# Optimization experiments

Hardware: AMD Instinct MI355X
Metric: run time of the kernel (lower is better)

## Reference

```python
import jax, jax.numpy as jnp
import numpy as np

B, TK, NK, H, E, V = 128, 400, 50, 256, 256, 50000


def setup_inputs() -> dict:
    key = jax.random.key(0)
    ks = iter(jax.random.split(key, 48))
    def rn(shape, s=1.0):
        return jax.random.normal(next(ks), shape, jnp.float32) * s
    def ru(shape):
        return jax.random.uniform(next(ks), shape, jnp.float32)
    z = lambda shape: jnp.zeros(shape, jnp.float32)
    s = 0.05
    inp = {}
    inp['y_t_1'] = jax.random.randint(next(ks), (B,), 0, V)
    inp['h_prev'] = rn((B, H))
    inp['c_prev'] = rn((B, H))
    inp['encoder_outputs'] = rn((B, TK, H))
    inp['encoder_outputs_node'] = rn((B, NK, H))
    inp['enc_padding_mask'] = jnp.ones((B, TK), jnp.float32)
    inp['enc_padding_mask_node'] = jnp.ones((B, NK), jnp.float32)
    inp['c_t_d'] = rn((B, H))
    inp['c_t_g'] = rn((B, H))
    inp['c_t_g2'] = rn((B, H))
    inp['coverage'] = z((B, TK))
    inp['flow'] = ru((B, NK))
    inp['node_to_token'] = ru((B, NK, TK))
    inp['graph'] = ru((B, NK, NK))
    inp['voc_d'] = jax.random.randint(next(ks), (B, TK), 0, V)
    inp['step'] = 0
    # learned parameters
    inp['emb_table'] = rn((V, E), s)
    inp['Wx'] = rn((4 * H, E), s); inp['bx'] = z((E,))
    inp['Wi'] = rn((E, 4 * H), s); inp['Wh'] = rn((H, 4 * H), s)
    inp['bi'] = z((4 * H,)); inp['bh'] = z((4 * H,))
    inp['Whd'] = rn((H, H), s); inp['Wsd'] = rn((2 * H, H), s)
    inp['wcd'] = rn((H,), s); inp['vd'] = rn((H,), s); inp['bd'] = z((H,))
    inp['Wn'] = rn((H, H), s); inp['Wsf'] = rn((2 * H, H), s)
    inp['vf'] = rn((H,), s); inp['bf'] = z((H,))
    inp['Wpg'] = rn((5 * H + E, 1), s); inp['bpg'] = z((1,))
    inp['W1'] = rn((4 * H, H), s); inp['b1'] = z((H,))
    inp['W2'] = rn((H, V), s); inp['b2'] = z((V,))
    return inp


def _forward(y_t_1, h_prev, c_prev, enc, enc_n, mask_t, mask_n, c_t_d, c_t_g, c_t_g2,
             coverage, flow, n2t, graph, voc_d, emb_table, Wx, bx, Wi, Wh, bi, bh,
             Whd, Wsd, wcd, vd, bd, Wn, Wsf, vf, bf, Wpg, bpg, W1, b1, W2, b2):
    sig, tanh = jax.nn.sigmoid, jnp.tanh
    y_emb = emb_table[y_t_1]                                   # [B,E]
    x = jnp.concatenate([c_t_d, c_t_g, c_t_g2, y_emb], 1) @ Wx + bx
    # single-step LSTM (torch gate order i,f,g,o)
    gates = x @ Wi + h_prev @ Wh + bi + bh
    gi, gf, gg, go = jnp.split(gates, 4, axis=1)
    c_new = sig(gf) * c_prev + sig(gi) * tanh(gg)
    h_new = sig(go) * tanh(c_new)
    s_hat = jnp.concatenate([h_new, c_new], 1)                 # [B,2H]
    # doc attention with coverage (Bahdanau)
    e = tanh(enc @ Whd + (s_hat @ Wsd)[:, None, :] + coverage[:, :, None] * wcd + bd) @ vd
    a = jax.nn.softmax(e, axis=1) * mask_t
    a = a / a.sum(1, keepdims=True)                            # [B,TK]
    c_d = jnp.einsum('bt,bth->bh', a, enc)
    coverage_next = coverage + a
    # event-graph node attention (flow-weighted, one-hop propagation)
    en = tanh(enc_n @ Wn + (s_hat @ Wsf)[:, None, :] + bf) @ vf
    an = jax.nn.softmax(en, axis=1) * mask_n
    an = an / an.sum(1, keepdims=True)
    an = an * flow
    an = an / an.sum(1, keepdims=True)                         # [B,NK]
    c_g = jnp.einsum('bn,bnh->bh', an, enc_n)
    an2 = jnp.einsum('bn,bnm->bm', an, graph) * mask_n
    an2 = an2 / an2.sum(1, keepdims=True)
    c_g2 = jnp.einsum('bn,bnh->bh', an2, enc_n)
    a_n2t = jnp.einsum('bn,bnt->bt', an, n2t)
    a_n2t = a_n2t / a_n2t.sum(1, keepdims=True)
    # flow update: per-node max of token attention restricted to node tokens
    flow_ = jnp.max(a[:, None, :] * n2t, axis=2)               # [B,NK]
    flow_next = flow_ / flow_.sum(1, keepdims=True)
    # pointer-generator gate
    p_gen = sig(jnp.concatenate([c_d, c_g, c_g2, s_hat, x], 1) @ Wpg + bpg)  # [B,1]
    out = jnp.concatenate([h_new, c_d, c_g, c_g2], 1) @ W1 + b1
    vocab_dist = jax.nn.softmax(out @ W2 + b2, axis=1)         # [B,V]
    attn_all = a / a.sum(1, keepdims=True)
    attn_ = (1.0 - p_gen) * attn_all
    vocab_ = p_gen * vocab_dist
    rows = jnp.arange(vocab_.shape[0])[:, None]
    final_dist = vocab_.at[rows, voc_d].add(attn_)             # scatter_add over vocab
    return (final_dist, (h_new, c_new), c_d, c_g, c_g2, a, a_n2t, p_gen,
            coverage_next, flow_next)


def reference(y_t_1, h_prev, c_prev, encoder_outputs, encoder_outputs_node,
              enc_padding_mask, enc_padding_mask_node, c_t_d, c_t_g, c_t_g2,
              coverage, flow, node_to_token, graph, voc_d, step,
              emb_table, Wx, bx, Wi, Wh, bi, bh, Whd, Wsd, wcd, vd, bd,
              Wn, Wsf, vf, bf, Wpg, bpg, W1, b1, W2, b2):
    return _forward(y_t_1, h_prev, c_prev, encoder_outputs, encoder_outputs_node,
                    enc_padding_mask, enc_padding_mask_node, c_t_d, c_t_g, c_t_g2,
                    coverage, flow, node_to_token, graph, voc_d, emb_table, Wx, bx,
                    Wi, Wh, bi, bh, Whd, Wsd, wcd, vd, bd, Wn, Wsf, vf, bf,
                    Wpg, bpg, W1, b1, W2, b2)
```

## Files before the change

kernel.cpp:

```cpp
#include <hip/hip_runtime.h>
#include <stdint.h>


typedef unsigned short u16;
typedef unsigned int   u32;

#define Bv  128
#define TKv 400
#define NKv 50
#define Hv  256
#define Vv  50000
#define VPAD 50176
#define NSv 16
#define CHUNKv 3136

typedef __attribute__((ext_vector_type(8))) short bf16x8;
typedef __attribute__((ext_vector_type(4))) float f32x4;

__device__ float g_x[32768];
__device__ float g_xp[4 * 32768];
__device__ float g_gates[131072];
__device__ float g_h[32768];
__device__ float g_c[32768];
__device__ float g_sdp[2 * 32768];
__device__ float g_sfp[2 * 32768];
__device__ float g_e[51200];
__device__ float g_en[6400];
__device__ float g_a[51200];
__device__ float g_cd[32768];
__device__ float g_cdp[2 * 32768];
__device__ float g_cg[32768];
__device__ float g_cg2[32768];
__device__ float g_pg[128];
__device__ float g_o1[32768];
__device__ float g_vred[Bv * NSv * 2];
__device__ float g_logits[6400000];
__device__ u16   g_Wdt[256 * 256];
__device__ u16   g_Wnt[256 * 256];
__device__ u16   g_W2t[(size_t)VPAD * 256];

__device__ __forceinline__ float sigm(float x) { return 1.f / (1.f + expf(-x)); }

__device__ __forceinline__ u16 f2bf(float f) {
    u32 u = __float_as_uint(f);
    return (u16)((u + 0x7fffu + ((u >> 16) & 1u)) >> 16);
}

__device__ __forceinline__ bf16x8 cvt8(const float* __restrict__ p) {
    const float4 a = *(const float4*)p;
    const float4 b = *(const float4*)(p + 4);
    bf16x8 r;
    r[0] = (short)f2bf(a.x); r[1] = (short)f2bf(a.y);
    r[2] = (short)f2bf(a.z); r[3] = (short)f2bf(a.w);
    r[4] = (short)f2bf(b.x); r[5] = (short)f2bf(b.y);
    r[6] = (short)f2bf(b.z); r[7] = (short)f2bf(b.w);
    return r;
}

__device__ __forceinline__ float fast_tanh(float x) {
    x = fminf(fmaxf(x, -15.f), 15.f);
    float e = __expf(2.f * x);
    return (e - 1.f) / (e + 1.f);
}

__device__ __forceinline__ void ms_merge(float& m1, float& s1, float m2, float s2) {
    float M = fmaxf(m1, m2);
    s1 = s1 * expf(m1 - M) + s2 * expf(m2 - M);
    m1 = M;
}

__global__ __launch_bounds__(256) void k_tc(
    const float* __restrict__ src, u16* __restrict__ dst, int K, int N)
{
    __shared__ float tile[32][33];
    const int n0 = blockIdx.x * 32, k0 = blockIdx.y * 32;
    const int tx = threadIdx.x & 31, ty = threadIdx.x >> 5;
    #pragma unroll
    for (int i = 0; i < 32; i += 8) {
        int k = k0 + ty + i, n = n0 + tx;
        tile[ty + i][tx] = (n < N) ? src[(size_t)k * N + n] : 0.f;
    }
    __syncthreads();
    #pragma unroll
    for (int i = 0; i < 32; i += 8) {
        int n = n0 + ty + i, k = k0 + tx;
        dst[(size_t)n * K + k] = f2bf(tile[tx][ty + i]);
    }
}

__global__ __launch_bounds__(256) void k_x(
    const int* __restrict__ y,
    const float* __restrict__ ctd, const float* __restrict__ ctg,
    const float* __restrict__ ctg2, const float* __restrict__ emb,
    const float* __restrict__ Wx)
{
    const int b = blockIdx.x, ks = blockIdx.y, j = threadIdx.x;
    __shared__ float cs[256];
    float v;
    if      (ks == 0) v = ctd [b * 256 + j];
    else if (ks == 1) v = ctg [b * 256 + j];
    else if (ks == 2) v = ctg2[b * 256 + j];
    else              v = emb[(size_t)y[b] * 256 + j];
    cs[j] = v;
    __syncthreads();

    float acc = 0.f;
    const float* w = Wx + (size_t)(ks * 256) * 256 + j;
    #pragma unroll 8
    for (int k = 0; k < 256; k++) acc += cs[k] * w[(size_t)k * 256];
    g_xp[ks * 32768 + b * 256 + j] = acc;
}

__global__ __launch_bounds__(256) void k_gates(
    const float* __restrict__ h_prev,
    const float* __restrict__ Wi, const float* __restrict__ Wh,
    const float* __restrict__ bi, const float* __restrict__ bh,
    const float* __restrict__ bx)
{
    const int b = blockIdx.x, cc = blockIdx.y, j = threadIdx.x;
    __shared__ float xs[256], hs[256];

    float xv = bx[j] + g_xp[b * 256 + j] + g_xp[32768 + b * 256 + j]
             + g_xp[65536 + b * 256 + j] + g_xp[98304 + b * 256 + j];
    xs[j] = xv;
    if (cc == 0) g_x[b * 256 + j] = xv;
    hs[j] = h_prev[b * 256 + j];
    __syncthreads();

    const int col = cc * 256 + j;
    float acc = bi[col] + bh[col];
    const float* wi = Wi + col;
    const float* wh = Wh + col;
    #pragma unroll 8
    for (int k = 0; k < 256; k++)
        acc += xs[k] * wi[(size_t)k * 1024] + hs[k] * wh[(size_t)k * 1024];
    g_gates[b * 1024 + col] = acc;
}

__global__ __launch_bounds__(256) void k_cellsd(
    const float* __restrict__ c_prev,
    const float* __restrict__ Wsd, const float* __restrict__ Wsf,
    float* __restrict__ out_h, float* __restrict__ out_c)
{
    const int b = blockIdx.x, ks = blockIdx.y, j = threadIdx.x;
    __shared__ float sh[256];

    const float* gb = g_gates + b * 1024;
    float gi_ = gb[j], gf_ = gb[256 + j], gg_ = gb[512 + j], go_ = gb[768 + j];
    float cp = c_prev[b * 256 + j];
    float cn = sigm(gf_) * cp + sigm(gi_) * tanhf(gg_);
    float hn = sigm(go_) * tanhf(cn);
    if (ks == 0) {
        g_h[b * 256 + j] = hn;  g_c[b * 256 + j] = cn;
        out_h[b * 256 + j] = hn; out_c[b * 256 + j] = cn;
    }
    sh[j] = (ks == 0) ? hn : cn;
    __syncthreads();

    float asd = 0.f, asf = 0.f;
    const float* wd = Wsd + (size_t)(ks * 256) * 256 + j;
    const float* wf = Wsf + (size_t)(ks * 256) * 256 + j;
    #pragma unroll 8
    for (int k = 0; k < 256; k++) {
        float sv = sh[k];
        asd += sv * wd[(size_t)k * 256];
        asf += sv * wf[(size_t)k * 256];
    }
    g_sdp[ks * 32768 + b * 256 + j] = asd;
    g_sfp[ks * 32768 + b * 256 + j] = asf;
}

__global__ __launch_bounds__(256) void k_scores(
    const float* __restrict__ src, int R,
    const u16* __restrict__ Wt,
    const float* __restrict__ addv0,
    const float* __restrict__ addv1,
    const float* __restrict__ abias,
    const float* __restrict__ cov,
    const float* __restrict__ wcw,
    const float* __restrict__ vv,
    float* __restrict__ eout)
{
    const int b = blockIdx.y, t0 = blockIdx.x * 64;
    const int tid = threadIdx.x;
    const int lane = tid & 63, wave = tid >> 6;
    const int nlow = lane & 15, quad = lane >> 4;
    const int trow = t0 + wave * 16 + nlow;
    const bool tval = trow < R;
    const float* arow = src + ((size_t)b * R + trow) * 256 + quad * 8;
    const u16* brow = Wt + nlow * 256 + quad * 8;

    const f32x4 zf = {0.f, 0.f, 0.f, 0.f};
    f32x4 acc[16];
    #pragma unroll
    for (int i = 0; i < 16; i++) acc[i] = zf;

    for (int k0 = 0; k0 < 256; k0 += 32) {
        bf16x8 af = {0, 0, 0, 0, 0, 0, 0, 0};
        if (tval) af = cvt8(arow + k0);
        #pragma unroll
        for (int nt = 0; nt < 16; nt++) {
            bf16x8 bf = *(const bf16x8*)(brow + nt * 4096 + k0);
            acc[nt] = __builtin_amdgcn_mfma_f32_16x16x32_bf16(af, bf, acc[nt], 0, 0, 0);
        }
    }

    float covt[4];
    #pragma unroll
    for (int r = 0; r < 4; r++) {
        int t = t0 + wave * 16 + quad * 4 + r;
        covt[r] = (cov && t < R) ? cov[b * R + t] : 0.f;
    }
    float s4[4] = {0.f, 0.f, 0.f, 0.f};
    #pragma unroll
    for (int nt = 0; nt < 16; nt++) {
        int col = nt * 16 + nlow;
        float vvc = vv[col];
        float adc = addv0[b * 256 + col] + addv1[b * 256 + col] + abias[col];
        float wcc = wcw ? wcw[col] : 0.f;
        #pragma unroll
        for (int r = 0; r < 4; r++)
            s4[r] += vvc * fast_tanh(acc[nt][r] + adc + covt[r] * wcc);
    }
    #pragma unroll
    for (int r = 0; r < 4; r++) {
        float s = s4[r];
        s += __shfl_xor(s, 1, 64);
        s += __shfl_xor(s, 2, 64);
        s += __shfl_xor(s, 4, 64);
        s += __shfl_xor(s, 8, 64);
        int t = t0 + wave * 16 + quad * 4 + r;
        if (nlow == 0 && t < R) eout[b * R + t] = s;
    }
}

__global__ __launch_bounds__(256) void k_doc(
    const float* __restrict__ mask,
    const float* __restrict__ cov,
    float* __restrict__ out_a, float* __restrict__ out_cov)
{
    const int b = blockIdx.x, tid = threadIdx.x;
    __shared__ float red[256];

    float e0 = g_e[b * TKv + tid];
    float e1 = (tid + 256 < TKv) ? g_e[b * TKv + tid + 256] : -1e30f;

    float m = fmaxf(e0, e1);
    red[tid] = m; __syncthreads();
    for (int s = 128; s > 0; s >>= 1) { if (tid < s) red[tid] = fmaxf(red[tid], red[tid + s]); __syncthreads(); }
    m = red[0]; __syncthreads();

    float p0 = expf(e0 - m) * mask[b * TKv + tid];
    float p1 = (tid + 256 < TKv) ? expf(e1 - m) * mask[b * TKv + tid + 256] : 0.f;
    red[tid] = p0 + p1; __syncthreads();
    for (int s = 128; s > 0; s >>= 1) { if (tid < s) red[tid] += red[tid + s]; __syncthreads(); }
    float inv = 1.f / red[0];

    float a0 = p0 * inv;
    g_a[b * TKv + tid] = a0;
    out_a[b * TKv + tid] = a0;
    out_cov[b * TKv + tid] = cov[b * TKv + tid] + a0;
    if (tid + 256 < TKv) {
        float a1 = p1 * inv;
        g_a[b * TKv + tid + 256] = a1;
        out_a[b * TKv + tid + 256] = a1;
        out_cov[b * TKv + tid + 256] = cov[b * TKv + tid + 256] + a1;
    }
}

__global__ __launch_bounds__(256) void k_cd(const float* __restrict__ enc)
{
    const int b = blockIdx.x, ks = blockIdx.y, tid = threadIdx.x;
    __shared__ float as_[200];
    if (tid < 200) as_[tid] = g_a[b * TKv + ks * 200 + tid];
    __syncthreads();

    const float* eb = enc + ((size_t)b * TKv + ks * 200) * 256 + tid;
    float acc = 0.f;
    #pragma unroll 8
    for (int t = 0; t < 200; t++) acc += as_[t] * eb[(size_t)t * 256];
    g_cdp[ks * 32768 + b * 256 + tid] = acc;
}

__global__ __launch_bounds__(256) void k_flow(
    const float* __restrict__ n2t, float* __restrict__ out_flow)
{
    const int b = blockIdx.x, tid = threadIdx.x;
    __shared__ float as_[TKv];
    __shared__ float fl[NKv];
    __shared__ float red[256];

    for (int t = tid; t < TKv; t += 256) as_[t] = g_a[b * TKv + t];
    __syncthreads();

    const int nn = tid >> 2, sub = tid & 3;
    float mx = 0.f;
    if (nn < NKv) {
        const float* nb = n2t + ((size_t)b * NKv + nn) * TKv + sub * 100;
        const float* ab = as_ + sub * 100;
        #pragma unroll 4
        for (int t = 0; t < 100; t++) mx = fmaxf(mx, ab[t] * nb[t]);
    }
    mx = fmaxf(mx, __shfl_xor(mx, 1, 64));
    mx = fmaxf(mx, __shfl_xor(mx, 2, 64));
    if (sub == 0 && nn < NKv) fl[nn] = mx;
    __syncthreads();

    float fv = (tid < NKv) ? fl[tid] : 0.f;
    red[tid] = fv; __syncthreads();
    for (int s = 128; s > 0; s >>= 1) { if (tid < s) red[tid] += red[tid + s]; __syncthreads(); }
    float fs = red[0];
    if (tid < NKv) out_flow[b * NKv + tid] = fl[tid] / fs;
}

__global__ __launch_bounds__(256) void k_node1(
    const float* __restrict__ encn,
    const float* __restrict__ maskn,
    const float* __restrict__ flow,
    const float* __restrict__ graph,
    const float* __restrict__ n2t,
    const float* __restrict__ Wpg, const float* __restrict__ bpg,
    float* __restrict__ out_cd, float* __restrict__ out_cg,
    float* __restrict__ out_cg2, float* __restrict__ out_ant,
    float* __restrict__ out_pgen)
{
    const int b = blockIdx.x, tid = threadIdx.x;
    __shared__ float ans[NKv], an2s[NKv], red[256];

    const float cd = g_cdp[b * 256 + tid] + g_cdp[32768 + b * 256 + tid];
    g_cd[b * 256 + tid] = cd;
    out_cd[b * 256 + tid] = cd;

    float v = (tid < NKv) ? g_en[b * NKv + tid] : -1e30f;
    red[tid] = v; __syncthreads();
    for (int s = 128; s > 0; s >>= 1) { if (tid < s) red[tid] = fmaxf(red[tid], red[tid + s]); __syncthreads(); }
    float m = red[0]; __syncthreads();

    float p = (tid < NKv) ? expf(v - m) * maskn[b * NKv + tid] : 0.f;
    red[tid] = p; __syncthreads();
    for (int s = 128; s > 0; s >>= 1) { if (tid < s) red[tid] += red[tid + s]; __syncthreads(); }
    float S = red[0]; __syncthreads();
    p = (tid < NKv) ? (p / S) * flow[b * NKv + tid] : 0.f;
    red[tid] = p; __syncthreads();
    for (int s = 128; s > 0; s >>= 1) { if (tid < s) red[tid] += red[tid + s]; __syncthreads(); }
    float S2 = red[0]; __syncthreads();
    if (tid < NKv) ans[tid] = p / S2;
    __syncthreads();

    float q = 0.f;
    if (tid < NKv) {
        const float* gb = graph + (size_t)b * NKv * NKv + tid;
        #pragma unroll
        for (int n = 0; n < NKv; n++) q += ans[n] * gb[n * NKv];
        q *= maskn[b * NKv + tid];
    }
    red[tid] = q; __syncthreads();
    for (int s = 128; s > 0; s >>= 1) { if (tid < s) red[tid] += red[tid + s]; __syncthreads(); }
    float S3 = red[0]; __syncthreads();
    if (tid < NKv) an2s[tid] = q / S3;
    __syncthreads();

    float cg = 0.f, cg2 = 0.f;
    {
        const float* enb = encn + (size_t)b * NKv * 256 + tid;
        #pragma unroll
        for (int n = 0; n < NKv; n++) {
            float e = enb[n * 256];
            cg  += ans[n]  * e;
            cg2 += an2s[n] * e;
        }
    }
    g_cg[b * 256 + tid] = cg;   out_cg[b * 256 + tid] = cg;
    g_cg2[b * 256 + tid] = cg2; out_cg2[b * 256 + tid] = cg2;

    float at0 = 0.f, at1 = 0.f;
    {
        const float* nb = n2t + (size_t)b * NKv * TKv;
        #pragma unroll
        for (int n = 0; n < NKv; n++) {
            float an = ans[n];
            at0 += an * nb[n * TKv + tid];
            if (tid + 256 < TKv) at1 += an * nb[n * TKv + tid + 256];
        }
    }
    float loc = at0 + ((tid + 256 < TKv) ? at1 : 0.f);
    red[tid] = loc; __syncthreads();
    for (int s = 128; s > 0; s >>= 1) { if (tid < s) red[tid] += red[tid + s]; __syncthreads(); }
    float S4 = red[0]; __syncthreads();
    out_ant[b * TKv + tid] = at0 / S4;
    if (tid + 256 < TKv) out_ant[b * TKv + tid + 256] = at1 / S4;

    float hvv = g_h[b * 256 + tid], cvv = g_c[b * 256 + tid];
    float xvv = g_x[b * 256 + tid];
    float part = cd  * Wpg[tid]        + cg  * Wpg[256 + tid]
               + cg2 * Wpg[512 + tid]  + hvv * Wpg[768 + tid]
               + cvv * Wpg[1024 + tid] + xvv * Wpg[1280 + tid];
    red[tid] = part; __syncthreads();
    for (int s = 128; s > 0; s >>= 1) { if (tid < s) red[tid] += red[tid + s]; __syncthreads(); }
    if (tid == 0) {
        float pg = sigm(red[0] + bpg[0]);
        g_pg[b] = pg; out_pgen[b] = pg;
    }
}

__global__ __launch_bounds__(256) void k_o1(
    const float* __restrict__ W1, const float* __restrict__ b1)
{
    const int b = blockIdx.x, cc = blockIdx.y, tid = threadIdx.x;
    __shared__ float cat[1024];
    __shared__ float red[256];

    cat[tid]       = g_h  [b * 256 + tid];
    cat[256 + tid] = g_cd [b * 256 + tid];
    cat[512 + tid] = g_cg [b * 256 + tid];
    cat[768 + tid] = g_cg2[b * 256 + tid];
    __syncthreads();

    const int lane = tid & 63, kq = tid >> 6;
    const int col = cc * 64 + lane;
    const float* w  = W1 + (size_t)(kq * 256) * 256 + col;
    const float* cs = cat + kq * 256;
    float acc = 0.f;
    #pragma unroll 8
    for (int k = 0; k < 256; k++) acc += cs[k] * w[(size_t)k * 256];
    red[tid] = acc; __syncthreads();

    if (tid < 64) {
        float o = b1[cc * 64 + tid]
                + red[tid] + red[64 + tid] + red[128 + tid] + red[192 + tid];
        g_o1[b * 256 + cc * 64 + tid] = o;
    }
}

__global__ __launch_bounds__(256) void k_logits(const float* __restrict__ b2)
{
    const int v0 = blockIdx.x * 128;
    const int tid = threadIdx.x;
    const int lane = tid & 63, wave = tid >> 6;
    const int nlow = lane & 15, quad = lane >> 4;

    const float* a0p = g_o1 + (wave * 32 + nlow) * 256 + quad * 8;
    const float* a1p = a0p + 16 * 256;
    const u16* bbase = g_W2t + (size_t)(v0 + nlow) * 256 + quad * 8;

    const f32x4 zf = {0.f, 0.f, 0.f, 0.f};
    f32x4 acc0[8], acc1[8];
    #pragma unroll
    for (int i = 0; i < 8; i++) { acc0[i] = zf; acc1[i] = zf; }

    for (int k0 = 0; k0 < 256; k0 += 32) {
        bf16x8 a0 = cvt8(a0p + k0);
        bf16x8 a1 = cvt8(a1p + k0);
        #pragma unroll
        for (int nt = 0; nt < 8; nt++) {
            bf16x8 bf = *(const bf16x8*)(bbase + (size_t)nt * 4096 + k0);
            acc0[nt] = __builtin_amdgcn_mfma_f32_16x16x32_bf16(a0, bf, acc0[nt], 0, 0, 0);
            acc1[nt] = __builtin_amdgcn_mfma_f32_16x16x32_bf16(a1, bf, acc1[nt], 0, 0, 0);
        }
    }

    #pragma unroll
    for (int nt = 0; nt < 8; nt++) {
        int v = v0 + nt * 16 + nlow;
        if (v < Vv) {
            float bb = b2[v];
            #pragma unroll
            for (int r = 0; r < 4; r++) {
                int row0 = wave * 32 + quad * 4 + r;
                g_logits[(size_t)row0 * Vv + v]        = acc0[nt][r] + bb;
                g_logits[(size_t)(row0 + 16) * Vv + v] = acc1[nt][r] + bb;
            }
        }
    }
}

__global__ __launch_bounds__(256) void k_vpart()
{
    const int b = blockIdx.x, ks = blockIdx.y, tid = threadIdx.x;
    __shared__ float rm[256], rs[256];

    const int base = ks * CHUNKv;
    const int end  = min(base + CHUNKv, Vv);
    const int n4   = (end - base) >> 2;
    const float4* L4 = (const float4*)(g_logits + (size_t)b * Vv + base);

    float m = -1e30f, s = 0.f;
    for (int i = tid; i < n4; i += 256) {
        float4 x = L4[i];
        float mx = fmaxf(fmaxf(x.x, x.y), fmaxf(x.z, x.w));
        if (mx > m) { s *= expf(m - mx); m = mx; }
        s += expf(x.x - m) + expf(x.y - m) + expf(x.z - m) + expf(x.w - m);
    }
    rm[tid] = m; rs[tid] = s; __syncthreads();
    for (int off = 128; off > 0; off >>= 1) {
        if (tid < off) {
            float m1 = rm[tid], s1 = rs[tid];
            ms_merge(m1, s1, rm[tid + off], rs[tid + off]);
            rm[tid] = m1; rs[tid] = s1;
        }
        __syncthreads();
    }
    if (tid == 0) {
        g_vred[(b * NSv + ks) * 2]     = rm[0];
        g_vred[(b * NSv + ks) * 2 + 1] = rs[0];
    }
}

__global__ __launch_bounds__(256) void k_vwrite(float* __restrict__ outF)
{
    const int b = blockIdx.x, ks = blockIdx.y, tid = threadIdx.x;

    float M = -1e30f, S = 0.f;
    #pragma unroll
    for (int i = 0; i < NSv; i++) {
        float mi = g_vred[(b * NSv + i) * 2];
        float si = g_vred[(b * NSv + i) * 2 + 1];
        ms_merge(M, S, mi, si);
    }
    const float inv = g_pg[b] / S;

    const int base = ks * CHUNKv;
    const int end  = min(base + CHUNKv, Vv);
    const int n4   = (end - base) >> 2;
    const float4* L4 = (const float4*)(g_logits + (size_t)b * Vv + base);
    float4* O4 = (float4*)(outF + (size_t)b * Vv + base);

    for (int i = tid; i < n4; i += 256) {
        float4 x = L4[i];
        float4 r;
        r.x = expf(x.x - M) * inv;
        r.y = expf(x.y - M) * inv;
        r.z = expf(x.z - M) * inv;
        r.w = expf(x.w - M) * inv;
        O4[i] = r;
    }
}

__global__ __launch_bounds__(256) void k_scatter(
    float* __restrict__ outF, const int* __restrict__ vocd)
{
    const int b = blockIdx.x, tid = threadIdx.x;
    float* Ob = outF + (size_t)b * Vv;
    const float omp = 1.f - g_pg[b];
    for (int t = tid; t < TKv; t += 256)
        atomicAdd(Ob + vocd[b * TKv + t], omp * g_a[b * TKv + t]);
}


extern "C" void kernel_launch(void* const* d_in, const int* in_sizes, int n_in,
                              void* d_out, int out_size, void* d_ws, size_t ws_size,
                              hipStream_t stream)
{
    (void)in_sizes; (void)n_in; (void)out_size; (void)d_ws; (void)ws_size;

    const int*   y      = (const int*)d_in[0];
    const float* h_prev = (const float*)d_in[1];
    const float* c_prev = (const float*)d_in[2];
    const float* enc    = (const float*)d_in[3];
    const float* encn   = (const float*)d_in[4];
    const float* mask   = (const float*)d_in[5];
    const float* maskn  = (const float*)d_in[6];
    const float* ctd    = (const float*)d_in[7];
    const float* ctg    = (const float*)d_in[8];
    const float* ctg2   = (const float*)d_in[9];
    const float* cov    = (const float*)d_in[10];
    const float* flow   = (const float*)d_in[11];
    const float* n2t    = (const float*)d_in[12];
    const float* graph  = (const float*)d_in[13];
    const int*   vocd   = (const int*)d_in[14];
    const float* emb    = (const float*)d_in[16];
    const float* Wx     = (const float*)d_in[17];
    const float* bx     = (const float*)d_in[18];
    const float* Wi     = (const float*)d_in[19];
    const float* Wh     = (const float*)d_in[20];
    const float* bi     = (const float*)d_in[21];
    const float* bh     = (const float*)d_in[22];
    const float* Whd    = (const float*)d_in[23];
    const float* Wsd    = (const float*)d_in[24];
    const float* wcdw   = (const float*)d_in[25];
    const float* vd     = (const float*)d_in[26];
    const float* bd     = (const float*)d_in[27];
    const float* Wn     = (const float*)d_in[28];
    const float* Wsf    = (const float*)d_in[29];
    const float* vf     = (const float*)d_in[30];
    const float* bfv    = (const float*)d_in[31];
    const float* Wpg    = (const float*)d_in[32];
    const float* bpg    = (const float*)d_in[33];
    const float* W1     = (const float*)d_in[34];
    const float* b1     = (const float*)d_in[35];
    const float* W2     = (const float*)d_in[36];
    const float* b2     = (const float*)d_in[37];

    float* o = (float*)d_out;
    float* o_final = o;
    float* o_h     = o + 6400000;
    float* o_c     = o + 6432768;
    float* o_cd    = o + 6465536;
    float* o_cg    = o + 6498304;
    float* o_cg2   = o + 6531072;
    float* o_a     = o + 6563840;
    float* o_ant   = o + 6615040;
    float* o_pg    = o + 6666240;
    float* o_cov   = o + 6666368;
    float* o_fl    = o + 6717568;

    float* g_e_p;   hipGetSymbolAddress((void**)&g_e_p,   HIP_SYMBOL(g_e));
    float* g_en_p;  hipGetSymbolAddress((void**)&g_en_p,  HIP_SYMBOL(g_en));
    float* g_sdp_p; hipGetSymbolAddress((void**)&g_sdp_p, HIP_SYMBOL(g_sdp));
    float* g_sfp_p; hipGetSymbolAddress((void**)&g_sfp_p, HIP_SYMBOL(g_sfp));
    u16*   g_Wdt_p; hipGetSymbolAddress((void**)&g_Wdt_p, HIP_SYMBOL(g_Wdt));
    u16*   g_Wnt_p; hipGetSymbolAddress((void**)&g_Wnt_p, HIP_SYMBOL(g_Wnt));
    u16*   g_W2t_p; hipGetSymbolAddress((void**)&g_W2t_p, HIP_SYMBOL(g_W2t));

    k_tc<<<dim3(8, 8), dim3(256), 0, stream>>>(Whd, g_Wdt_p, 256, 256);
    k_tc<<<dim3(8, 8), dim3(256), 0, stream>>>(Wn,  g_Wnt_p, 256, 256);
    k_tc<<<dim3(VPAD / 32, 8), dim3(256), 0, stream>>>(W2, g_W2t_p, 256, Vv);

    k_x<<<dim3(Bv, 4), dim3(256), 0, stream>>>(y, ctd, ctg, ctg2, emb, Wx);

    k_gates<<<dim3(Bv, 4), dim3(256), 0, stream>>>(h_prev, Wi, Wh, bi, bh, bx);

    k_cellsd<<<dim3(Bv, 2), dim3(256), 0, stream>>>(c_prev, Wsd, Wsf, o_h, o_c);

    k_scores<<<dim3(7, Bv), dim3(256), 0, stream>>>(
        enc, TKv, g_Wdt_p, g_sdp_p, g_sdp_p + 32768, bd, cov, wcdw, vd, g_e_p);

    k_scores<<<dim3(1, Bv), dim3(256), 0, stream>>>(
        encn, NKv, g_Wnt_p, g_sfp_p, g_sfp_p + 32768, bfv,
        nullptr, nullptr, vf, g_en_p);

    k_doc<<<dim3(Bv), dim3(256), 0, stream>>>(mask, cov, o_a, o_cov);

    k_cd<<<dim3(Bv, 2), dim3(256), 0, stream>>>(enc);

    k_flow<<<dim3(Bv), dim3(256), 0, stream>>>(n2t, o_fl);

    k_node1<<<dim3(Bv), dim3(256), 0, stream>>>(
        encn, maskn, flow, graph, n2t, Wpg, bpg,
        o_cd, o_cg, o_cg2, o_ant, o_pg);

    k_o1<<<dim3(Bv, 4), dim3(256), 0, stream>>>(W1, b1);

    k_logits<<<dim3(VPAD / 128), dim3(256), 0, stream>>>(b2);

    k_vpart<<<dim3(Bv, NSv), dim3(256), 0, stream>>>();

    k_vwrite<<<dim3(Bv, NSv), dim3(256), 0, stream>>>(o_final);

    k_scatter<<<dim3(Bv), dim3(256), 0, stream>>>(o_final, vocd);
}
```

Before: 543.5 us.

## Retile attention score MFMA as 4x4 register tile and halve logits block width

The attention score kernel now gives each wave a 64-column slice of the hidden dimension across all 64 rows, using a 4x4 register tile of MFMA accumulators. A/B fragments are reused four times each per k-step, replacing one A fragment reused across sixteen B loads. Partial v-dot sums from each wave are combined through shared memory before the write. Separately, the logits kernel covers 64 vocab columns per block instead of 128, doubling the grid to improve occupancy and load balance, at the cost of rereading the activation rows more often.

```diff
diff --git a/kernel.cpp b/kernel.cpp
--- a/kernel.cpp
+++ b/kernel.cpp
@@ -185,52 +185,78 @@
     const int tid = threadIdx.x;
     const int lane = tid & 63, wave = tid >> 6;
     const int nlow = lane & 15, quad = lane >> 4;
-    const int trow = t0 + wave * 16 + nlow;
-    const bool tval = trow < R;
-    const float* arow = src + ((size_t)b * R + trow) * 256 + quad * 8;
-    const u16* brow = Wt + nlow * 256 + quad * 8;
+
+    const u16* brow = Wt + (size_t)(wave * 64 + nlow) * 256 + quad * 8;
+
+    bool tval[4]; const float* arow[4];
+    #pragma unroll
+    for (int mi = 0; mi < 4; mi++) {
+        int trow = t0 + mi * 16 + nlow;
+        tval[mi] = trow < R;
+        arow[mi] = src + ((size_t)b * R + trow) * 256 + quad * 8;
+    }
 
     const f32x4 zf = {0.f, 0.f, 0.f, 0.f};
-    f32x4 acc[16];
-    #pragma unroll
-    for (int i = 0; i < 16; i++) acc[i] = zf;
+    f32x4 acc[4][4];
+    #pragma unroll
+    for (int mi = 0; mi < 4; mi++)
+        #pragma unroll
+        for (int ni = 0; ni < 4; ni++) acc[mi][ni] = zf;
 
     for (int k0 = 0; k0 < 256; k0 += 32) {
-        bf16x8 af = {0, 0, 0, 0, 0, 0, 0, 0};
-        if (tval) af = cvt8(arow + k0);
-        #pragma unroll
-        for (int nt = 0; nt < 16; nt++) {
-            bf16x8 bf = *(const bf16x8*)(brow + nt * 4096 + k0);
-            acc[nt] = __builtin_amdgcn_mfma_f32_16x16x32_bf16(af, bf, acc[nt], 0, 0, 0);
-        }
-    }
-
-    float covt[4];
-    #pragma unroll
-    for (int r = 0; r < 4; r++) {
-        int t = t0 + wave * 16 + quad * 4 + r;
-        covt[r] = (cov && t < R) ? cov[b * R + t] : 0.f;
-    }
-    float s4[4] = {0.f, 0.f, 0.f, 0.f};
-    #pragma unroll
-    for (int nt = 0; nt < 16; nt++) {
-        int col = nt * 16 + nlow;
-        float vvc = vv[col];
-        float adc = addv0[b * 256 + col] + addv1[b * 256 + col] + abias[col];
-        float wcc = wcw ? wcw[col] : 0.f;
-        #pragma unroll
-        for (int r = 0; r < 4; r++)
-            s4[r] += vvc * fast_tanh(acc[nt][r] + adc + covt[r] * wcc);
-    }
-    #pragma unroll
-    for (int r = 0; r < 4; r++) {
-        float s = s4[r];
-        s += __shfl_xor(s, 1, 64);
-        s += __shfl_xor(s, 2, 64);
-        s += __shfl_xor(s, 4, 64);
-        s += __shfl_xor(s, 8, 64);
-        int t = t0 + wave * 16 + quad * 4 + r;
-        if (nlow == 0 && t < R) eout[b * R + t] = s;
+        bf16x8 af[4], bf[4];
+        #pragma unroll
+        for (int mi = 0; mi < 4; mi++) {
+            af[mi] = (bf16x8){0, 0, 0, 0, 0, 0, 0, 0};
+            if (tval[mi]) af[mi] = cvt8(arow[mi] + k0);
+        }
+        #pragma unroll
+        for (int ni = 0; ni < 4; ni++)
+            bf[ni] = *(const bf16x8*)(brow + ni * 4096 + k0);
+        #pragma unroll
+        for (int mi = 0; mi < 4; mi++)
+            #pragma unroll
+            for (int ni = 0; ni < 4; ni++)
+                acc[mi][ni] = __builtin_amdgcn_mfma_f32_16x16x32_bf16(
+                    af[mi], bf[ni], acc[mi][ni], 0, 0, 0);
+    }
+
+    __shared__ float part[4][64];
+    #pragma unroll
+    for (int mi = 0; mi < 4; mi++) {
+        float covt[4];
+        #pragma unroll
+        for (int r = 0; r < 4; r++) {
+            int t = t0 + mi * 16 + quad * 4 + r;
+            covt[r] = (cov && t < R) ? cov[b * R + t] : 0.f;
+        }
+        float s4[4] = {0.f, 0.f, 0.f, 0.f};
+        #pragma unroll
+        for (int ni = 0; ni < 4; ni++) {
+            int col = wave * 64 + ni * 16 + nlow;
+            float vvc = vv[col];
+            float adc = addv0[b * 256 + col] + addv1[b * 256 + col] + abias[col];
+            float wcc = wcw ? wcw[col] : 0.f;
+            #pragma unroll
+            for (int r = 0; r < 4; r++)
+                s4[r] += vvc * fast_tanh(acc[mi][ni][r] + adc + covt[r] * wcc);
+        }
+        #pragma unroll
+        for (int r = 0; r < 4; r++) {
+            float s = s4[r];
+            s += __shfl_xor(s, 1, 64);
+            s += __shfl_xor(s, 2, 64);
+            s += __shfl_xor(s, 4, 64);
+            s += __shfl_xor(s, 8, 64);
+            if (nlow == 0) part[wave][mi * 16 + quad * 4 + r] = s;
+        }
+    }
+    __syncthreads();
+    if (tid < 64) {
+        int t = t0 + tid;
+        if (t < R)
+            eout[b * R + t] =
+                part[0][tid] + part[1][tid] + part[2][tid] + part[3][tid];
     }
 }
 
@@ -434,7 +460,7 @@
 
 __global__ __launch_bounds__(256) void k_logits(const float* __restrict__ b2)
 {
-    const int v0 = blockIdx.x * 128;
+    const int v0 = blockIdx.x * 64;
     const int tid = threadIdx.x;
     const int lane = tid & 63, wave = tid >> 6;
     const int nlow = lane & 15, quad = lane >> 4;
@@ -444,15 +470,15 @@
     const u16* bbase = g_W2t + (size_t)(v0 + nlow) * 256 + quad * 8;
 
     const f32x4 zf = {0.f, 0.f, 0.f, 0.f};
-    f32x4 acc0[8], acc1[8];
-    #pragma unroll
-    for (int i = 0; i < 8; i++) { acc0[i] = zf; acc1[i] = zf; }
+    f32x4 acc0[4], acc1[4];
+    #pragma unroll
+    for (int i = 0; i < 4; i++) { acc0[i] = zf; acc1[i] = zf; }
 
     for (int k0 = 0; k0 < 256; k0 += 32) {
         bf16x8 a0 = cvt8(a0p + k0);
         bf16x8 a1 = cvt8(a1p + k0);
         #pragma unroll
-        for (int nt = 0; nt < 8; nt++) {
+        for (int nt = 0; nt < 4; nt++) {
             bf16x8 bf = *(const bf16x8*)(bbase + (size_t)nt * 4096 + k0);
             acc0[nt] = __builtin_amdgcn_mfma_f32_16x16x32_bf16(a0, bf, acc0[nt], 0, 0, 0);
             acc1[nt] = __builtin_amdgcn_mfma_f32_16x16x32_bf16(a1, bf, acc1[nt], 0, 0, 0);
@@ -460,7 +486,7 @@
     }
 
     #pragma unroll
-    for (int nt = 0; nt < 8; nt++) {
+    for (int nt = 0; nt < 4; nt++) {
         int v = v0 + nt * 16 + nlow;
         if (v < Vv) {
             float bb = b2[v];
@@ -641,7 +667,7 @@
 
     k_o1<<<dim3(Bv, 4), dim3(256), 0, stream>>>(W1, b1);
 
-    k_logits<<<dim3(VPAD / 128), dim3(256), 0, stream>>>(b2);
+    k_logits<<<dim3(VPAD / 64), dim3(256), 0, stream>>>(b2);
 
     k_vpart<<<dim3(Bv, NSv), dim3(256), 0, stream>>>();
 
```

Measured after the change: 529.6 us. -2.6%, faster.
